# Optimization experiments

Hardware: AMD Instinct MI355X
Metric: run time of the kernel (lower is better)

The kernel has to match this reference:

```python
import jax, jax.numpy as jnp
import numpy as np

B, NV, NQ, NA = 128, 100, 14, 10
V_DIM, Q_DIM, A_DIM = 2048, 1024, 1024
H_DIM, RANK, HD, G = 512, 32, 16, 2  # HD = H_DIM // RANK, G = glimpse


def setup_inputs() -> dict:
    key = jax.random.key(0)
    ks = jax.random.split(key, 16)
    s = 0.05
    return {
        "v": jax.random.normal(ks[0], (B, NV, V_DIM), jnp.float32),
        "q": jax.random.normal(ks[1], (B, NQ, Q_DIM), jnp.float32),
        "a": jax.random.normal(ks[2], (B, NA, A_DIM), jnp.float32),
        # tucker projections (FCNet = Linear + ReLU; dropout identity at eval)
        "Wv": jax.random.normal(ks[3], (H_DIM, V_DIM), jnp.float32) * s,
        "bv": jnp.zeros((H_DIM,), jnp.float32),
        "Wq": jax.random.normal(ks[4], (H_DIM, Q_DIM), jnp.float32) * s,
        "bq": jnp.zeros((H_DIM,), jnp.float32),
        "Wa": jax.random.normal(ks[5], (H_DIM, A_DIM), jnp.float32) * s,
        "ba": jnp.zeros((H_DIM,), jnp.float32),
        # rank-wise projection nets, stacked over rank: [rank, HD, H_DIM]
        "Wvr": jax.random.normal(ks[6], (RANK, HD, H_DIM), jnp.float32) * s,
        "bvr": jnp.zeros((RANK, HD), jnp.float32),
        "Wqr": jax.random.normal(ks[7], (RANK, HD, H_DIM), jnp.float32) * s,
        "bqr": jnp.zeros((RANK, HD), jnp.float32),
        "War": jax.random.normal(ks[8], (RANK, HD, H_DIM), jnp.float32) * s,
        "bar": jnp.zeros((RANK, HD), jnp.float32),
        # Tucker core T_g with h_out squeezed: [rank, hv, hq, ha, glimpse]
        "T": jax.random.normal(ks[9], (RANK, HD, HD, HD, G), jnp.float32),
    }


def reference(v, q, a, Wv, bv, Wq, bq, Wa, ba, Wvr, bvr, Wqr, bqr, War, bar, T):
    relu = jax.nn.relu
    # modality tucker projections: [B, N, H_DIM]
    vt = relu(jnp.einsum('bnd,hd->bnh', v, Wv) + bv)
    qt = relu(jnp.einsum('bnd,hd->bnh', q, Wq) + bq)
    at = relu(jnp.einsum('bnd,hd->bnh', a, Wa) + ba)
    # rank-wise FCNets, batched over rank: [B, rank, N, HD]
    v_ = relu(jnp.einsum('bnh,rch->brnc', vt, Wvr) + bvr[None, :, None, :])
    q_ = relu(jnp.einsum('bnh,rch->brnc', qt, Wqr) + bqr[None, :, None, :])
    a_ = relu(jnp.einsum('bnh,rch->brnc', at, War) + bar[None, :, None, :])
    # 6-way Tucker contraction, summed over rank: [B, NV, NQ, NA, G]
    f_emb = jnp.einsum('rijkg,bnvi,bnqj,bnak->bvqag', T, v_, q_, a_,
                       optimize=True)
    return f_emb
```

## Files before the change

kernel.cpp:

```cpp
#include <hip/hip_runtime.h>
#include <cstddef>
#include <cstdint>

#define B_    128
#define NV_   100
#define NQ_   14
#define NA_   10
#define HDIM  512
#define RANK_ 32
#define HD_   16
#define G_    2

typedef __bf16 bf16x8 __attribute__((ext_vector_type(8)));
typedef float  f32x4  __attribute__((ext_vector_type(4)));
union Frag { uint4 u; bf16x8 v; };

__device__ __forceinline__ unsigned int f2bf(float f) {
  unsigned int u = __float_as_uint(f);
  u = (u + 0x7FFFu + ((u >> 16) & 1u)) >> 16;
  return u & 0xFFFFu;
}

__global__ __launch_bounds__(256) void cvt_kernel(
    const float* __restrict__ s0, const float* __restrict__ s1,
    const float* __restrict__ s2, const float* __restrict__ s3,
    const float* __restrict__ s4, const float* __restrict__ s5,
    const float* __restrict__ s6, const float* __restrict__ s7,
    unsigned short* __restrict__ dst)
{
  const int pref[8] = {896, 1536, 2048, 2304, 2560, 2688, 2816, 2944};
  const float* srcs[8] = {s0, s1, s2, s3, s4, s5, s6, s7};
  const int blk = blockIdx.x;
  int seg = 0;
  #pragma unroll
  for (int i = 0; i < 7; ++i) if (blk >= pref[i]) seg = i + 1;
  const int base_chunk = seg ? pref[seg - 1] : 0;
  const size_t loc = (size_t)(blk - base_chunk) * 2048 + threadIdx.x * 8;
  const float* s = srcs[seg] + loc;
  float4 f0 = *(const float4*)s;
  float4 f1 = *(const float4*)(s + 4);
  ushort4 o0, o1;
  o0.x = f2bf(f0.x); o0.y = f2bf(f0.y); o0.z = f2bf(f0.z); o0.w = f2bf(f0.w);
  o1.x = f2bf(f1.x); o1.y = f2bf(f1.y); o1.z = f2bf(f1.z); o1.w = f2bf(f1.w);
  unsigned short* d = dst + (size_t)blk * 2048 + threadIdx.x * 8;
  *(ushort4*)d = o0;
  *(ushort4*)(d + 4) = o1;
}

__global__ __launch_bounds__(256) void l1_gemm(
    const float* __restrict__ v,
    const unsigned short* __restrict__ qb, const unsigned short* __restrict__ ab,
    const unsigned short* __restrict__ Wvb, const unsigned short* __restrict__ Wqb,
    const unsigned short* __restrict__ Wab,
    const float* __restrict__ bv, const float* __restrict__ bq,
    const float* __restrict__ ba,
    unsigned short* __restrict__ vtb, unsigned short* __restrict__ qtb,
    unsigned short* __restrict__ atb)
{
  __shared__ __align__(16) unsigned short As[2048];
  __shared__ __align__(16) unsigned short Bs[4096];
  const int bx = blockIdx.x;
  int grp, gx, gy, K;
  const unsigned short *A16 = qb, *W;
  const float* bias;
  unsigned short* C;
  if (bx < 800) {
    grp = 0; const int xcd = bx & 7; const int j = bx >> 3;
    gy = xcd * 25 + (j >> 2); gx = j & 3;
    W = Wvb; bias = bv; C = vtb; K = 2048;
  } else if (bx < 912) {
    grp = 1; const int lo = bx - 800; gy = lo >> 2; gx = lo & 3;
    A16 = qb; W = Wqb; bias = bq; C = qtb; K = 1024;
  } else {
    grp = 2; const int lo = bx - 912; gy = lo >> 2; gx = lo & 3;
    A16 = ab; W = Wab; bias = ba; C = atb; K = 1024;
  }
  const int bm = gy * 64, bn = gx * 128;
  const int t = threadIdx.x;
  const int w = t >> 6, l = t & 63;
  const int wm = (w >> 1) * 32, wn = (w & 1) * 64;
  const int rr = l >> 2, ko = (l & 3) * 8;

  f32x4 acc[2][4];
  #pragma unroll
  for (int i = 0; i < 2; ++i)
    #pragma unroll
    for (int j = 0; j < 4; ++j) acc[i][j] = f32x4{0.f, 0.f, 0.f, 0.f};

  if (grp == 0) {
    const int row = t >> 2, koff = (t & 3) * 8;
    for (int k0 = 0; k0 < 2048; k0 += 32) {
      const float* src = v + (size_t)(bm + row) * 2048 + k0 + koff;
      float4 f0 = *(const float4*)(src + 0);
      float4 f1 = *(const float4*)(src + 4);
      #pragma unroll
      for (int c2 = 0; c2 < 2; ++c2) {
        const int c = w * 2 + c2;
        const unsigned short* gpB = W + (size_t)(bn + c * 16 + rr) * 2048 + k0 + ko;
        __builtin_amdgcn_global_load_lds(
            (const __attribute__((address_space(1))) void*)gpB,
            (__attribute__((address_space(3))) void*)&Bs[c * 512], 16, 0, 0);
      }
      uint4 p;
      p.x = f2bf(f0.x) | (f2bf(f0.y) << 16);
      p.y = f2bf(f0.z) | (f2bf(f0.w) << 16);
      p.z = f2bf(f1.x) | (f2bf(f1.y) << 16);
      p.w = f2bf(f1.z) | (f2bf(f1.w) << 16);
      *(uint4*)&As[row * 32 + koff] = p;
      __syncthreads();
      Frag fa[2], fb[4];
      #pragma unroll
      for (int i = 0; i < 2; ++i)
        fa[i].u = *(const uint4*)&As[(wm + 16 * i + (l & 15)) * 32 + (l >> 4) * 8];
      #pragma unroll
      for (int j = 0; j < 4; ++j)
        fb[j].u = *(const uint4*)&Bs[(wn + 16 * j + (l & 15)) * 32 + (l >> 4) * 8];
      #pragma unroll
      for (int i = 0; i < 2; ++i)
        #pragma unroll
        for (int j = 0; j < 4; ++j)
          acc[i][j] = __builtin_amdgcn_mfma_f32_16x16x32_bf16(fa[i].v, fb[j].v, acc[i][j], 0, 0, 0);
      __syncthreads();
    }
  } else {
    for (int k0 = 0; k0 < K; k0 += 32) {
      {
        const unsigned short* gpA = A16 + (size_t)(bm + w * 16 + rr) * K + k0 + ko;
        __builtin_amdgcn_global_load_lds(
            (const __attribute__((address_space(1))) void*)gpA,
            (__attribute__((address_space(3))) void*)&As[w * 512], 16, 0, 0);
      }
      #pragma unroll
      for (int c2 = 0; c2 < 2; ++c2) {
        const int c = w * 2 + c2;
        const unsigned short* gpB = W + (size_t)(bn + c * 16 + rr) * K + k0 + ko;
        __builtin_amdgcn_global_load_lds(
            (const __attribute__((address_space(1))) void*)gpB,
            (__attribute__((address_space(3))) void*)&Bs[c * 512], 16, 0, 0);
      }
      __syncthreads();
      Frag fa[2], fb[4];
      #pragma unroll
      for (int i = 0; i < 2; ++i)
        fa[i].u = *(const uint4*)&As[(wm + 16 * i + (l & 15)) * 32 + (l >> 4) * 8];
      #pragma unroll
      for (int j = 0; j < 4; ++j)
        fb[j].u = *(const uint4*)&Bs[(wn + 16 * j + (l & 15)) * 32 + (l >> 4) * 8];
      #pragma unroll
      for (int i = 0; i < 2; ++i)
        #pragma unroll
        for (int j = 0; j < 4; ++j)
          acc[i][j] = __builtin_amdgcn_mfma_f32_16x16x32_bf16(fa[i].v, fb[j].v, acc[i][j], 0, 0, 0);
      __syncthreads();
    }
  }

  const int q4 = (l >> 4) * 4, cl = l & 15;
  #pragma unroll
  for (int i = 0; i < 2; ++i)
    #pragma unroll
    for (int j = 0; j < 4; ++j) {
      const int col = bn + wn + 16 * j + cl;
      const float bs = bias[col];
      #pragma unroll
      for (int r = 0; r < 4; ++r) {
        const int row = bm + wm + 16 * i + q4 + r;
        float o = fmaxf(acc[i][j][r] + bs, 0.f);
        C[(size_t)row * 512 + col] = (unsigned short)f2bf(o);
      }
    }
}

__global__ __launch_bounds__(256) void l2_gemm(
    const unsigned short* __restrict__ vtb, const unsigned short* __restrict__ qtb,
    const unsigned short* __restrict__ atb,
    const unsigned short* __restrict__ Wvrb, const unsigned short* __restrict__ Wqrb,
    const unsigned short* __restrict__ Warb,
    const float* __restrict__ bvr, const float* __restrict__ bqr,
    const float* __restrict__ bar,
    unsigned short* __restrict__ vrb, float* __restrict__ q_r, float* __restrict__ a_r)
{
  __shared__ __align__(16) unsigned short As[2048];
  __shared__ __align__(16) unsigned short Bs[4096];
  const int bx = blockIdx.x;
  int grp, gx, gy;
  const unsigned short *A16, *W;
  const float* bias;
  if (bx < 800) {
    grp = 0; const int xcd = bx & 7; const int j = bx >> 3;
    gy = xcd * 25 + (j >> 2); gx = j & 3;
    A16 = vtb; W = Wvrb; bias = bvr;
  } else if (bx < 912) {
    grp = 1; const int lo = bx - 800; gy = lo >> 2; gx = lo & 3;
    A16 = qtb; W = Wqrb; bias = bqr;
  } else {
    grp = 2; const int lo = bx - 912; gy = lo >> 2; gx = lo & 3;
    A16 = atb; W = Warb; bias = bar;
  }
  const int bm = gy * 64, bn = gx * 128;
  const int t = threadIdx.x;
  const int w = t >> 6, l = t & 63;
  const int wm = (w >> 1) * 32, wn = (w & 1) * 64;
  const int rr = l >> 2, ko = (l & 3) * 8;

  f32x4 acc[2][4];
  #pragma unroll
  for (int i = 0; i < 2; ++i)
    #pragma unroll
    for (int j = 0; j < 4; ++j) acc[i][j] = f32x4{0.f, 0.f, 0.f, 0.f};

  for (int k0 = 0; k0 < 512; k0 += 32) {
    {
      const unsigned short* gpA = A16 + (size_t)(bm + w * 16 + rr) * 512 + k0 + ko;
      __builtin_amdgcn_global_load_lds(
          (const __attribute__((address_space(1))) void*)gpA,
          (__attribute__((address_space(3))) void*)&As[w * 512], 16, 0, 0);
    }
    #pragma unroll
    for (int c2 = 0; c2 < 2; ++c2) {
      const int c = w * 2 + c2;
      const unsigned short* gpB = W + (size_t)(bn + c * 16 + rr) * 512 + k0 + ko;
      __builtin_amdgcn_global_load_lds(
          (const __attribute__((address_space(1))) void*)gpB,
          (__attribute__((address_space(3))) void*)&Bs[c * 512], 16, 0, 0);
    }
    __syncthreads();
    Frag fa[2], fb[4];
    #pragma unroll
    for (int i = 0; i < 2; ++i)
      fa[i].u = *(const uint4*)&As[(wm + 16 * i + (l & 15)) * 32 + (l >> 4) * 8];
    #pragma unroll
    for (int j = 0; j < 4; ++j)
      fb[j].u = *(const uint4*)&Bs[(wn + 16 * j + (l & 15)) * 32 + (l >> 4) * 8];
    #pragma unroll
    for (int i = 0; i < 2; ++i)
      #pragma unroll
      for (int j = 0; j < 4; ++j)
        acc[i][j] = __builtin_amdgcn_mfma_f32_16x16x32_bf16(fa[i].v, fb[j].v, acc[i][j], 0, 0, 0);
    __syncthreads();
  }

  const int q4 = (l >> 4) * 4, cl = l & 15;
  #pragma unroll
  for (int i = 0; i < 2; ++i)
    #pragma unroll
    for (int j = 0; j < 4; ++j) {
      const int col = bn + wn + 16 * j + cl;
      const float bs = bias[col];
      #pragma unroll
      for (int r = 0; r < 4; ++r) {
        const int row = bm + wm + 16 * i + q4 + r;
        float o = fmaxf(acc[i][j][r] + bs, 0.f);
        if (grp == 0)      vrb[(size_t)row * 512 + col] = (unsigned short)f2bf(o);
        else if (grp == 1) q_r[(size_t)row * 512 + col] = o;
        else               a_r[(size_t)row * 512 + col] = o;
      }
    }
}

__global__ void tsum_kernel(const float* __restrict__ T, float* __restrict__ Tsum)
{
  const int idx = blockIdx.x * 256 + threadIdx.x;
  float s = 0.f;
  #pragma unroll
  for (int r = 0; r < RANK_; ++r) s += T[r * 8192 + idx];
  Tsum[idx] = s;
}

__global__ __launch_bounds__(256) void build_w_kernel(
    const float* __restrict__ q_, const float* __restrict__ a_,
    const float* __restrict__ Tsum, unsigned short* __restrict__ WmatT)
{
  const int n = blockIdx.x, b = blockIdx.y, t = threadIdx.x;
  __shared__ float Ts[8192];
  __shared__ float U[14 * 544];

  #pragma unroll
  for (int s = 0; s < 8; ++s)
    ((float4*)Ts)[s * 256 + t] = ((const float4*)Tsum)[s * 256 + t];
  __syncthreads();

  {
    const int i = t >> 4, k = t & 15;
    float acc0[NQ_], acc1[NQ_];
    #pragma unroll
    for (int q = 0; q < NQ_; ++q) { acc0[q] = 0.f; acc1[q] = 0.f; }
    const float* qbase = q_ + (size_t)b * NQ_ * HDIM + n * 16;
    #pragma unroll
    for (int j = 0; j < 16; ++j) {
      float2 ts = *(const float2*)&Ts[i * 512 + j * 32 + k * 2];
      #pragma unroll
      for (int q = 0; q < NQ_; ++q) {
        float qv = qbase[q * HDIM + j];
        acc0[q] += ts.x * qv;
        acc1[q] += ts.y * qv;
      }
    }
    #pragma unroll
    for (int q = 0; q < NQ_; ++q) {
      float2 uu; uu.x = acc0[q]; uu.y = acc1[q];
      *(float2*)&U[q * 544 + i * 34 + k * 2] = uu;
    }
  }
  __syncthreads();

  if ((t >> 4) < NQ_) {
    const int q = t >> 4, i = t & 15;
    float acc0[NA_], acc1[NA_];
    #pragma unroll
    for (int a = 0; a < NA_; ++a) { acc0[a] = 0.f; acc1[a] = 0.f; }
    const float* abase = a_ + (size_t)b * NA_ * HDIM + n * 16;
    #pragma unroll
    for (int k = 0; k < 16; ++k) {
      float2 uu = *(const float2*)&U[q * 544 + i * 34 + k * 2];
      #pragma unroll
      for (int a = 0; a < NA_; ++a) {
        float av = abase[a * HDIM + k];
        acc0[a] += uu.x * av;
        acc1[a] += uu.y * av;
      }
    }
    unsigned short* wb = WmatT + (size_t)b * 320 * 512 + (n * 16 + i);
    #pragma unroll
    for (int a = 0; a < NA_; ++a) {
      wb[(size_t)((q * 10 + a) * 2 + 0) * 512] = (unsigned short)f2bf(acc0[a]);
      wb[(size_t)((q * 10 + a) * 2 + 1) * 512] = (unsigned short)f2bf(acc1[a]);
    }
  }
}

__global__ __launch_bounds__(256) void final_mfma(
    const unsigned short* __restrict__ Vrb, const unsigned short* __restrict__ WmatT,
    float* __restrict__ out)
{
  __shared__ __align__(16) unsigned short As[2048];
  __shared__ __align__(16) unsigned short Bs[5120];
  const int b  = blockIdx.y;
  const int mh = blockIdx.x >> 1;
  const int n0 = (blockIdx.x & 1) * 160;
  const int t = threadIdx.x;
  const int w = t >> 6, l = t & 63;
  const int wm = (w >> 1) * 32;
  const int wn = (w & 1) * 80;

  f32x4 acc[2][5];
  #pragma unroll
  for (int mi = 0; mi < 2; ++mi)
    #pragma unroll
    for (int nj = 0; nj < 5; ++nj) acc[mi][nj] = f32x4{0.f, 0.f, 0.f, 0.f};

  const unsigned short* Wb = WmatT + (size_t)b * 320 * 512;

  for (int k0 = 0; k0 < 512; k0 += 32) {
    {
      int grow = b * NV_ + mh * 64 + w * 16 + (l >> 2);
      if (grow > B_ * NV_ - 1) grow = B_ * NV_ - 1;
      const unsigned short* src = Vrb + (size_t)grow * HDIM + k0 + (l & 3) * 8;
      __builtin_amdgcn_global_load_lds(
          (const __attribute__((address_space(1))) void*)src,
          (__attribute__((address_space(3))) void*)&As[w * 512], 16, 0, 0);
    }
    #pragma unroll
    for (int c = 0; c < 3; ++c) {
      const int base = c * 256 + w * 64;
      if (base < 640) {
        const int li = base + l;
        const int nrow = li >> 2, ko2 = (li & 3) * 8;
        const unsigned short* src = Wb + (size_t)(n0 + nrow) * 512 + k0 + ko2;
        __builtin_amdgcn_global_load_lds(
            (const __attribute__((address_space(1))) void*)src,
            (__attribute__((address_space(3))) void*)&Bs[base * 8], 16, 0, 0);
      }
    }
    __syncthreads();

    Frag fa[2], fb[5];
    #pragma unroll
    for (int mi = 0; mi < 2; ++mi)
      fa[mi].u = *(const uint4*)&As[(wm + mi * 16 + (l & 15)) * 32 + (l >> 4) * 8];
    #pragma unroll
    for (int nj = 0; nj < 5; ++nj)
      fb[nj].u = *(const uint4*)&Bs[(wn + nj * 16 + (l & 15)) * 32 + (l >> 4) * 8];
    #pragma unroll
    for (int mi = 0; mi < 2; ++mi)
      #pragma unroll
      for (int nj = 0; nj < 5; ++nj)
        acc[mi][nj] = __builtin_amdgcn_mfma_f32_16x16x32_bf16(fa[mi].v, fb[nj].v, acc[mi][nj], 0, 0, 0);
    __syncthreads();
  }

  #pragma unroll
  for (int mi = 0; mi < 2; ++mi)
    #pragma unroll
    for (int nj = 0; nj < 5; ++nj) {
      const int col = n0 + wn + nj * 16 + (l & 15);
      if (col < 280) {
        #pragma unroll
        for (int r = 0; r < 4; ++r) {
          const int row = mh * 64 + wm + mi * 16 + (l >> 4) * 4 + r;
          if (row < NV_)
            out[((size_t)b * NV_ + row) * 280 + col] = acc[mi][nj][r];
        }
      }
    }
}

extern "C" void kernel_launch(void* const* d_in, const int* in_sizes, int n_in,
                              void* d_out, int out_size, void* d_ws, size_t ws_size,
                              hipStream_t stream)
{
  const float* v   = (const float*)d_in[0];
  const float* q   = (const float*)d_in[1];
  const float* a   = (const float*)d_in[2];
  const float* Wv  = (const float*)d_in[3];
  const float* bv  = (const float*)d_in[4];
  const float* Wq  = (const float*)d_in[5];
  const float* bq  = (const float*)d_in[6];
  const float* Wa  = (const float*)d_in[7];
  const float* ba  = (const float*)d_in[8];
  const float* Wvr = (const float*)d_in[9];
  const float* bvr = (const float*)d_in[10];
  const float* Wqr = (const float*)d_in[11];
  const float* bqr = (const float*)d_in[12];
  const float* War = (const float*)d_in[13];
  const float* bar = (const float*)d_in[14];
  const float* T   = (const float*)d_in[15];

  unsigned short* wsu = (unsigned short*)d_ws;
  float* wsf = (float*)d_ws;

  unsigned short* WmatT = wsu;
  unsigned short* qb    = wsu;
  unsigned short* ab    = wsu + 1835008;
  unsigned short* Wvb   = wsu + 3145728;
  unsigned short* Wqb   = wsu + 4194304;
  unsigned short* Wab   = wsu + 4718592;
  unsigned short* Wvrb  = wsu + 5242880;
  unsigned short* Wqrb  = wsu + 5505024;
  unsigned short* Warb  = wsu + 5767168;
  unsigned short* vtb   = wsu + 20971520;
  unsigned short* qtb   = wsu + 27525120;
  unsigned short* atb   = wsu + 28442624;
  unsigned short* vrb   = wsu + 29097984;
  float* q_r  = wsf + 17825792;
  float* a_r  = wsf + 18743296;
  float* Tsum = wsf + 19398656;

  cvt_kernel<<<2944, 256, 0, stream>>>(q, a, Wv, Wq, Wa, Wvr, Wqr, War, wsu);

  l1_gemm<<<992, 256, 0, stream>>>(v, qb, ab, Wvb, Wqb, Wab, bv, bq, ba,
                                   vtb, qtb, atb);
  l2_gemm<<<992, 256, 0, stream>>>(vtb, qtb, atb, Wvrb, Wqrb, Warb,
                                   bvr, bqr, bar, vrb, q_r, a_r);

  tsum_kernel<<<32, 256, 0, stream>>>(T, Tsum);
  build_w_kernel<<<dim3(32, 128), 256, 0, stream>>>(q_r, a_r, Tsum, WmatT);
  final_mfma<<<dim3(4, 128), 256, 0, stream>>>(vrb, WmatT, (float*)d_out);
}
```

Measured before the change: 357.8 us.

## Use 128x128x64 double-buffered swizzled LDS tiles in projection GEMMs

Both projection GEMM kernels move from 64x128 tiles with K-step 32 and single-buffered LDS to 128x128 tiles with K-step 64. LDS is now double-buffered, so the next tile's global-to-LDS loads, and the fp32 v register loads, are issued before the current tile's MFMAs, with one barrier per step. An XOR swizzle on the LDS layout avoids bank conflicts. The grid is halved to 496 blocks, which gives more reuse per block but fewer blocks to fill the GPU, adds register pressure from the larger accumulator and the v prefetch, and uses 64KB of LDS per block.

New measurement: 347.5 us. 1.03x faster.

```diff
diff --git a/kernel.cpp b/kernel.cpp
--- a/kernel.cpp
+++ b/kernel.cpp
@@ -47,7 +47,27 @@
   *(ushort4*)(d + 4) = o1;
 }
 
-__global__ __launch_bounds__(256) void l1_gemm(
+__device__ __forceinline__ void stage_swz(const unsigned short* __restrict__ src,
+                                          int K, unsigned short* dst, int t)
+{
+  const int w64 = t & 192;
+  const int l = t & 63;
+  #pragma unroll
+  for (int i = 0; i < 4; ++i) {
+    const int sb = i * 256 + w64;
+    const int li = sb + l;
+    const int row = li >> 3;
+    const int p = li & 7;
+    const int s = p ^ (row & 7);
+    const unsigned short* gp = src + (size_t)row * K + s * 8;
+    unsigned short* dp = dst + sb * 8;
+    __builtin_amdgcn_global_load_lds(
+        (const __attribute__((address_space(1))) void*)gp,
+        (__attribute__((address_space(3))) void*)dp, 16, 0, 0);
+  }
+}
+
+__global__ __launch_bounds__(256, 2) void l1_gemm(
     const float* __restrict__ v,
     const unsigned short* __restrict__ qb, const unsigned short* __restrict__ ab,
     const unsigned short* __restrict__ Wvb, const unsigned short* __restrict__ Wqb,
@@ -57,107 +77,114 @@
     unsigned short* __restrict__ vtb, unsigned short* __restrict__ qtb,
     unsigned short* __restrict__ atb)
 {
-  __shared__ __align__(16) unsigned short As[2048];
-  __shared__ __align__(16) unsigned short Bs[4096];
+  __shared__ __align__(16) unsigned short As[2][8192];
+  __shared__ __align__(16) unsigned short Bs[2][8192];
   const int bx = blockIdx.x;
   int grp, gx, gy, K;
   const unsigned short *A16 = qb, *W;
   const float* bias;
   unsigned short* C;
-  if (bx < 800) {
-    grp = 0; const int xcd = bx & 7; const int j = bx >> 3;
-    gy = xcd * 25 + (j >> 2); gx = j & 3;
-    W = Wvb; bias = bv; C = vtb; K = 2048;
-  } else if (bx < 912) {
-    grp = 1; const int lo = bx - 800; gy = lo >> 2; gx = lo & 3;
+  if (bx < 400) {
+    grp = 0; const int xcd = bx & 7, j = bx >> 3; const int m = xcd * 50 + j;
+    gy = m >> 2; gx = m & 3; W = Wvb; bias = bv; C = vtb; K = 2048;
+  } else if (bx < 456) {
+    grp = 1; const int lo = bx - 400; gy = lo >> 2; gx = lo & 3;
     A16 = qb; W = Wqb; bias = bq; C = qtb; K = 1024;
   } else {
-    grp = 2; const int lo = bx - 912; gy = lo >> 2; gx = lo & 3;
+    grp = 2; const int lo = bx - 456; gy = lo >> 2; gx = lo & 3;
     A16 = ab; W = Wab; bias = ba; C = atb; K = 1024;
   }
-  const int bm = gy * 64, bn = gx * 128;
+  const int nsteps = K >> 6;
+  const int bm = gy * 128, bn = gx * 128;
   const int t = threadIdx.x;
   const int w = t >> 6, l = t & 63;
-  const int wm = (w >> 1) * 32, wn = (w & 1) * 64;
-  const int rr = l >> 2, ko = (l & 3) * 8;
-
-  f32x4 acc[2][4];
-  #pragma unroll
-  for (int i = 0; i < 2; ++i)
+  const int wm = (w >> 1) * 64, wn = (w & 1) * 64;
+
+  f32x4 acc[4][4];
+  #pragma unroll
+  for (int i = 0; i < 4; ++i)
     #pragma unroll
     for (int j = 0; j < 4; ++j) acc[i][j] = f32x4{0.f, 0.f, 0.f, 0.f};
 
+  const int ar = t >> 1, kh = t & 1;
+  const float* vrow = (grp == 0)
+      ? v + (size_t)(bm + ar) * 2048 + kh * 32 : (const float*)nullptr;
+
+  stage_swz(W + (size_t)bn * K, K, Bs[0], t);
   if (grp == 0) {
-    const int row = t >> 2, koff = (t & 3) * 8;
-    for (int k0 = 0; k0 < 2048; k0 += 32) {
-      const float* src = v + (size_t)(bm + row) * 2048 + k0 + koff;
-      float4 f0 = *(const float4*)(src + 0);
-      float4 f1 = *(const float4*)(src + 4);
-      #pragma unroll
-      for (int c2 = 0; c2 < 2; ++c2) {
-        const int c = w * 2 + c2;
-        const unsigned short* gpB = W + (size_t)(bn + c * 16 + rr) * 2048 + k0 + ko;
-        __builtin_amdgcn_global_load_lds(
-            (const __attribute__((address_space(1))) void*)gpB,
-            (__attribute__((address_space(3))) void*)&Bs[c * 512], 16, 0, 0);
-      }
+    float4 f[8];
+    #pragma unroll
+    for (int i = 0; i < 8; ++i) f[i] = ((const float4*)vrow)[i];
+    unsigned short* abp = &As[0][ar * 64];
+    #pragma unroll
+    for (int s2 = 0; s2 < 4; ++s2) {
       uint4 p;
-      p.x = f2bf(f0.x) | (f2bf(f0.y) << 16);
-      p.y = f2bf(f0.z) | (f2bf(f0.w) << 16);
-      p.z = f2bf(f1.x) | (f2bf(f1.y) << 16);
-      p.w = f2bf(f1.z) | (f2bf(f1.w) << 16);
-      *(uint4*)&As[row * 32 + koff] = p;
-      __syncthreads();
-      Frag fa[2], fb[4];
-      #pragma unroll
-      for (int i = 0; i < 2; ++i)
-        fa[i].u = *(const uint4*)&As[(wm + 16 * i + (l & 15)) * 32 + (l >> 4) * 8];
-      #pragma unroll
-      for (int j = 0; j < 4; ++j)
-        fb[j].u = *(const uint4*)&Bs[(wn + 16 * j + (l & 15)) * 32 + (l >> 4) * 8];
-      #pragma unroll
-      for (int i = 0; i < 2; ++i)
+      p.x = f2bf(f[2*s2].x)   | (f2bf(f[2*s2].y)   << 16);
+      p.y = f2bf(f[2*s2].z)   | (f2bf(f[2*s2].w)   << 16);
+      p.z = f2bf(f[2*s2+1].x) | (f2bf(f[2*s2+1].y) << 16);
+      p.w = f2bf(f[2*s2+1].z) | (f2bf(f[2*s2+1].w) << 16);
+      const int sx = (kh * 4 + s2) ^ (ar & 7);
+      *(uint4*)&abp[sx * 8] = p;
+    }
+  } else {
+    stage_swz(A16 + (size_t)bm * K, K, As[0], t);
+  }
+  __syncthreads();
+
+  for (int step = 0; step < nsteps; ++step) {
+    const int db = step & 1;
+    const bool hn = (step + 1) < nsteps;
+    const int k0n = (step + 1) << 6;
+    float4 f[8];
+    if (hn) {
+      stage_swz(W + (size_t)bn * K + k0n, K, Bs[db ^ 1], t);
+      if (grp == 0) {
+        #pragma unroll
+        for (int i = 0; i < 8; ++i) f[i] = ((const float4*)(vrow + k0n))[i];
+      } else {
+        stage_swz(A16 + (size_t)bm * K + k0n, K, As[db ^ 1], t);
+      }
+    }
+    const unsigned short* Ad = As[db];
+    const unsigned short* Bd = Bs[db];
+    #pragma unroll
+    for (int ks = 0; ks < 2; ++ks) {
+      Frag fa[4], fb[4];
+      #pragma unroll
+      for (int i = 0; i < 4; ++i) {
+        const int r = wm + 16 * i + (l & 15);
+        fa[i].u = *(const uint4*)&Ad[r * 64 + (((ks * 4 + (l >> 4)) ^ (r & 7)) * 8)];
+      }
+      #pragma unroll
+      for (int j = 0; j < 4; ++j) {
+        const int r = wn + 16 * j + (l & 15);
+        fb[j].u = *(const uint4*)&Bd[r * 64 + (((ks * 4 + (l >> 4)) ^ (r & 7)) * 8)];
+      }
+      #pragma unroll
+      for (int i = 0; i < 4; ++i)
         #pragma unroll
         for (int j = 0; j < 4; ++j)
           acc[i][j] = __builtin_amdgcn_mfma_f32_16x16x32_bf16(fa[i].v, fb[j].v, acc[i][j], 0, 0, 0);
-      __syncthreads();
-    }
-  } else {
-    for (int k0 = 0; k0 < K; k0 += 32) {
-      {
-        const unsigned short* gpA = A16 + (size_t)(bm + w * 16 + rr) * K + k0 + ko;
-        __builtin_amdgcn_global_load_lds(
-            (const __attribute__((address_space(1))) void*)gpA,
-            (__attribute__((address_space(3))) void*)&As[w * 512], 16, 0, 0);
-      }
-      #pragma unroll
-      for (int c2 = 0; c2 < 2; ++c2) {
-        const int c = w * 2 + c2;
-        const unsigned short* gpB = W + (size_t)(bn + c * 16 + rr) * K + k0 + ko;
-        __builtin_amdgcn_global_load_lds(
-            (const __attribute__((address_space(1))) void*)gpB,
-            (__attribute__((address_space(3))) void*)&Bs[c * 512], 16, 0, 0);
-      }
-      __syncthreads();
-      Frag fa[2], fb[4];
-      #pragma unroll
-      for (int i = 0; i < 2; ++i)
-        fa[i].u = *(const uint4*)&As[(wm + 16 * i + (l & 15)) * 32 + (l >> 4) * 8];
-      #pragma unroll
-      for (int j = 0; j < 4; ++j)
-        fb[j].u = *(const uint4*)&Bs[(wn + 16 * j + (l & 15)) * 32 + (l >> 4) * 8];
-      #pragma unroll
-      for (int i = 0; i < 2; ++i)
-        #pragma unroll
-        for (int j = 0; j < 4; ++j)
-          acc[i][j] = __builtin_amdgcn_mfma_f32_16x16x32_bf16(fa[i].v, fb[j].v, acc[i][j], 0, 0, 0);
-      __syncthreads();
-    }
+    }
+    if (hn && grp == 0) {
+      unsigned short* abp = &As[db ^ 1][ar * 64];
+      #pragma unroll
+      for (int s2 = 0; s2 < 4; ++s2) {
+        uint4 p;
+        p.x = f2bf(f[2*s2].x)   | (f2bf(f[2*s2].y)   << 16);
+        p.y = f2bf(f[2*s2].z)   | (f2bf(f[2*s2].w)   << 16);
+        p.z = f2bf(f[2*s2+1].x) | (f2bf(f[2*s2+1].y) << 16);
+        p.w = f2bf(f[2*s2+1].z) | (f2bf(f[2*s2+1].w) << 16);
+        const int sx = (kh * 4 + s2) ^ (ar & 7);
+        *(uint4*)&abp[sx * 8] = p;
+      }
+    }
+    __syncthreads();
   }
 
   const int q4 = (l >> 4) * 4, cl = l & 15;
   #pragma unroll
-  for (int i = 0; i < 2; ++i)
+  for (int i = 0; i < 4; ++i)
     #pragma unroll
     for (int j = 0; j < 4; ++j) {
       const int col = bn + wn + 16 * j + cl;
@@ -171,7 +198,7 @@
     }
 }
 
-__global__ __launch_bounds__(256) void l2_gemm(
+__global__ __launch_bounds__(256, 2) void l2_gemm(
     const unsigned short* __restrict__ vtb, const unsigned short* __restrict__ qtb,
     const unsigned short* __restrict__ atb,
     const unsigned short* __restrict__ Wvrb, const unsigned short* __restrict__ Wqrb,
@@ -180,69 +207,72 @@
     const float* __restrict__ bar,
     unsigned short* __restrict__ vrb, float* __restrict__ q_r, float* __restrict__ a_r)
 {
-  __shared__ __align__(16) unsigned short As[2048];
-  __shared__ __align__(16) unsigned short Bs[4096];
+  __shared__ __align__(16) unsigned short As[2][8192];
+  __shared__ __align__(16) unsigned short Bs[2][8192];
   const int bx = blockIdx.x;
   int grp, gx, gy;
   const unsigned short *A16, *W;
   const float* bias;
-  if (bx < 800) {
-    grp = 0; const int xcd = bx & 7; const int j = bx >> 3;
-    gy = xcd * 25 + (j >> 2); gx = j & 3;
-    A16 = vtb; W = Wvrb; bias = bvr;
-  } else if (bx < 912) {
-    grp = 1; const int lo = bx - 800; gy = lo >> 2; gx = lo & 3;
+  if (bx < 400) {
+    grp = 0; const int xcd = bx & 7, j = bx >> 3; const int m = xcd * 50 + j;
+    gy = m >> 2; gx = m & 3; A16 = vtb; W = Wvrb; bias = bvr;
+  } else if (bx < 456) {
+    grp = 1; const int lo = bx - 400; gy = lo >> 2; gx = lo & 3;
     A16 = qtb; W = Wqrb; bias = bqr;
   } else {
-    grp = 2; const int lo = bx - 912; gy = lo >> 2; gx = lo & 3;
+    grp = 2; const int lo = bx - 456; gy = lo >> 2; gx = lo & 3;
     A16 = atb; W = Warb; bias = bar;
   }
-  const int bm = gy * 64, bn = gx * 128;
+  const int bm = gy * 128, bn = gx * 128;
   const int t = threadIdx.x;
   const int w = t >> 6, l = t & 63;
-  const int wm = (w >> 1) * 32, wn = (w & 1) * 64;
-  const int rr = l >> 2, ko = (l & 3) * 8;
-
-  f32x4 acc[2][4];
-  #pragma unroll
-  for (int i = 0; i < 2; ++i)
+  const int wm = (w >> 1) * 64, wn = (w & 1) * 64;
+
+  f32x4 acc[4][4];
+  #pragma unroll
+  for (int i = 0; i < 4; ++i)
     #pragma unroll
     for (int j = 0; j < 4; ++j) acc[i][j] = f32x4{0.f, 0.f, 0.f, 0.f};
 
-  for (int k0 = 0; k0 < 512; k0 += 32) {
-    {
-      const unsigned short* gpA = A16 + (size_t)(bm + w * 16 + rr) * 512 + k0 + ko;
-      __builtin_amdgcn_global_load_lds(
-          (const __attribute__((address_space(1))) void*)gpA,
-          (__attribute__((address_space(3))) void*)&As[w * 512], 16, 0, 0);
-    }
-    #pragma unroll
-    for (int c2 = 0; c2 < 2; ++c2) {
-      const int c = w * 2 + c2;
-      const unsigned short* gpB = W + (size_t)(bn + c * 16 + rr) * 512 + k0 + ko;
-      __builtin_amdgcn_global_load_lds(
-          (const __attribute__((address_space(1))) void*)gpB,
-          (__attribute__((address_space(3))) void*)&Bs[c * 512], 16, 0, 0);
+  stage_swz(W + (size_t)bn * 512, 512, Bs[0], t);
+  stage_swz(A16 + (size_t)bm * 512, 512, As[0], t);
+  __syncthreads();
+
+  for (int step = 0; step < 8; ++step) {
+    const int db = step & 1;
+    const bool hn = (step + 1) < 8;
+    const int k0n = (step + 1) << 6;
+    if (hn) {
+      stage_swz(W + (size_t)bn * 512 + k0n, 512, Bs[db ^ 1], t);
+      stage_swz(A16 + (size_t)bm * 512 + k0n, 512, As[db ^ 1], t);
+    }
+    const unsigned short* Ad = As[db];
+    const unsigned short* Bd = Bs[db];
+    #pragma unroll
+    for (int ks = 0; ks < 2; ++ks) {
+      Frag fa[4], fb[4];
+      #pragma unroll
+      for (int i = 0; i < 4; ++i) {
+        const int r = wm + 16 * i + (l & 15);
+        fa[i].u = *(const uint4*)&Ad[r * 64 + (((ks * 4 + (l >> 4)) ^ (r & 7)) * 8)];
+      }
+      #pragma unroll
+      for (int j = 0; j < 4; ++j) {
+        const int r = wn + 16 * j + (l & 15);
+        fb[j].u = *(const uint4*)&Bd[r * 64 + (((ks * 4 + (l >> 4)) ^ (r & 7)) * 8)];
+      }
+      #pragma unroll
+      for (int i = 0; i < 4; ++i)
+        #pragma unroll
+        for (int j = 0; j < 4; ++j)
+          acc[i][j] = __builtin_amdgcn_mfma_f32_16x16x32_bf16(fa[i].v, fb[j].v, acc[i][j], 0, 0, 0);
     }
     __syncthreads();
-    Frag fa[2], fb[4];
-    #pragma unroll
-    for (int i = 0; i < 2; ++i)
-      fa[i].u = *(const uint4*)&As[(wm + 16 * i + (l & 15)) * 32 + (l >> 4) * 8];
-    #pragma unroll
-    for (int j = 0; j < 4; ++j)
-      fb[j].u = *(const uint4*)&Bs[(wn + 16 * j + (l & 15)) * 32 + (l >> 4) * 8];
-    #pragma unroll
-    for (int i = 0; i < 2; ++i)
-      #pragma unroll
-      for (int j = 0; j < 4; ++j)
-        acc[i][j] = __builtin_amdgcn_mfma_f32_16x16x32_bf16(fa[i].v, fb[j].v, acc[i][j], 0, 0, 0);
-    __syncthreads();
   }
 
   const int q4 = (l >> 4) * 4, cl = l & 15;
   #pragma unroll
-  for (int i = 0; i < 2; ++i)
+  for (int i = 0; i < 4; ++i)
     #pragma unroll
     for (int j = 0; j < 4; ++j) {
       const int col = bn + wn + 16 * j + cl;
@@ -448,9 +478,9 @@
 
   cvt_kernel<<<2944, 256, 0, stream>>>(q, a, Wv, Wq, Wa, Wvr, Wqr, War, wsu);
 
-  l1_gemm<<<992, 256, 0, stream>>>(v, qb, ab, Wvb, Wqb, Wab, bv, bq, ba,
+  l1_gemm<<<496, 256, 0, stream>>>(v, qb, ab, Wvb, Wqb, Wab, bv, bq, ba,
                                    vtb, qtb, atb);
-  l2_gemm<<<992, 256, 0, stream>>>(vtb, qtb, atb, Wvrb, Wqrb, Warb,
+  l2_gemm<<<496, 256, 0, stream>>>(vtb, qtb, atb, Wvrb, Wqrb, Warb,
                                    bvr, bqr, bar, vrb, q_r, a_r);
 
   tsum_kernel<<<32, 256, 0, stream>>>(T, Tsum);
```
